# Kernel optimization log

Hardware: AMD Instinct MI355X
Metric: run time of the kernel (lower is better)

Reference implementation:

```python
import jax, jax.numpy as jnp
import numpy as np

EPS = 1e-5  # F.layer_norm default eps
H = 0.1     # step size h

def mm1(K, x):
    # 1x1 conv1d == channel matmul: K [O,I], x [B,I,M] -> [B,O,M]
    return jnp.einsum('oi,bim->bom', K, x)

def full_ln(x):
    # F.layer_norm(x, x.shape): normalize over ALL elements (incl. batch)
    m = jnp.mean(x)
    v = jnp.mean((x - m) ** 2)
    return (x - m) / jnp.sqrt(v + EPS)

def setup_inputs() -> dict:
    key = jax.random.key(0)
    ks = jax.random.split(key, 12)
    B, nNin, nEin = 1, 16, 16
    nNopen = nEopen = nEhid = nNclose = nEclose = 64
    nlayer, N, E = 4, 20000, 320000
    stdv, stdvp = 0.01, 0.001
    NEf = 2 * nNopen + nEopen   # 192
    Nnf = 2 * nEhid + nNopen    # 192
    return {
        'xn': jax.random.normal(ks[0], (B, nNin, N), jnp.float32),
        'xe': jax.random.normal(ks[1], (B, nEin, E), jnp.float32),
        'iInd': jax.random.randint(ks[2], (E,), 0, N, jnp.int32),
        'jInd': jax.random.randint(ks[3], (E,), 0, N, jnp.int32),
        'KNopen': jax.random.normal(ks[4], (nNopen, nNin), jnp.float32) * stdv,
        'KEopen': jax.random.normal(ks[5], (nEopen, nEin), jnp.float32) * stdv,
        'KNclose': jax.random.normal(ks[6], (nNclose, nNopen), jnp.float32) * stdv,
        'KEclose': jax.random.normal(ks[7], (nEclose, nEopen), jnp.float32) * stdv,
        'KE1': jax.random.uniform(ks[8], (nlayer, nEhid, NEf), jnp.float32) * stdvp,
        'KE2': jax.random.uniform(ks[9], (nlayer, nEhid, nEhid), jnp.float32) * stdvp,
        'KE3': jax.random.uniform(ks[10], (nlayer, nEopen, nEhid), jnp.float32) * stdvp,
        'KN': jax.random.uniform(ks[11], (nlayer, nNopen, Nnf), jnp.float32) * stdvp,
    }

def reference(xn, xe, iInd, jInd, KNopen, KEopen, KNclose, KEclose, KE1, KE2, KE3, KN):
    N = xn.shape[-1]
    xn = mm1(KNopen, xn)
    xe = mm1(KEopen, xe)
    nlayers = KE1.shape[0]
    for i in range(nlayers):
        xi = xn[:, :, iInd]
        xj = xn[:, :, jInd]
        gradX = xi - xj               # Graph.nodeGrad
        intX = 0.5 * (xi + xj)        # Graph.nodeAve
        xec = jnp.concatenate([intX, xe, gradX], axis=1)   # [B, 2*nNopen+nEopen, E]
        xec = jax.nn.relu(full_ln(mm1(KE1[i], xec)))
        xec = jax.nn.relu(full_ln(mm1(KE2[i], xec)))
        z = jnp.zeros(xec.shape[:2] + (N,), xec.dtype)
        divXe = z.at[:, :, iInd].add(xec).at[:, :, jInd].add(-xec)          # Graph.edgeDiv
        intXe = 0.5 * z.at[:, :, iInd].add(xec).at[:, :, jInd].add(xec)     # Graph.edgeAve
        xnc = jnp.concatenate([intXe, xn, divXe], axis=1)   # [B, 2*nEhid+nNopen, N]
        xe = xe + H * mm1(KE3[i], xec)
        xn = xn + H * mm1(KN[i], xnc)
    xn = mm1(KNclose, xn)
    xe = mm1(KEclose, xe)
    return (xn, xe)
```

## Files before the change

kernel.cpp:

```cpp
#include <hip/hip_runtime.h>
#include <math.h>

#define H_COEF 0.1f
#define LN_EPS 1e-5

__device__ __forceinline__ int lds_idx(int c, int el) {
  return (c << 8) + (el ^ c);
}

__device__ __forceinline__ void stat_reduce(float s, float ss, double* stat) {
#pragma unroll
  for (int off = 32; off > 0; off >>= 1) {
    s += __shfl_down(s, off);
    ss += __shfl_down(ss, off);
  }
  __shared__ float bs[8], bss[8];
  const int wid = threadIdx.x >> 6;
  const int lane = threadIdx.x & 63;
  if (lane == 0) { bs[wid] = s; bss[wid] = ss; }
  __syncthreads();
  if (threadIdx.x == 0) {
    float S = 0.f, SS = 0.f;
    const int nw = blockDim.x >> 6;
    for (int w = 0; w < nw; w++) { S += bs[w]; SS += bss[w]; }
    atomicAdd(stat, (double)S);
    atomicAdd(stat + 1, (double)SS);
  }
}

__global__ __launch_bounds__(256) void prep_weights_kernel(
    const float* __restrict__ KE1, const float* __restrict__ KN,
    const float* __restrict__ KNopen, const float* __restrict__ KNclose,
    float* __restrict__ WUT, float* __restrict__ WVT, float* __restrict__ WNaT,
    float* __restrict__ WNbT, float* __restrict__ WNcT,
    float* __restrict__ WNopT, float* __restrict__ WNclT, int nlayer) {
  const int idx = blockIdx.x * blockDim.x + threadIdx.x;
  const int total = nlayer * 4096;
  if (idx < total) {
    const int l = idx >> 12;
    const int r = idx & 4095;
    const int k = r >> 6;
    const int c = r & 63;
    const float a = KE1[(size_t)l * 12288 + c * 192 + k];
    const float g = KE1[(size_t)l * 12288 + c * 192 + 128 + k];
    WUT[idx] = 0.5f * a + g;
    WVT[idx] = 0.5f * a - g;
    WNaT[idx] = KN[(size_t)l * 12288 + c * 192 + k];
    WNbT[idx] = KN[(size_t)l * 12288 + c * 192 + 64 + k];
    WNcT[idx] = KN[(size_t)l * 12288 + c * 192 + 128 + k];
  }
  if (idx < 4096) {
    const int k = idx >> 6;
    const int c = idx & 63;
    WNclT[idx] = KNclose[c * 64 + k];
    if (k < 16) WNopT[k * 64 + c] = KNopen[c * 16 + k];
  }
}

__global__ __launch_bounds__(256) void hist_kernel(
    const int* __restrict__ iInd, const int* __restrict__ jInd,
    int* __restrict__ cnt_i, int* __restrict__ cnt_j, int E) {
  const int e = blockIdx.x * blockDim.x + threadIdx.x;
  if (e < E) {
    atomicAdd(&cnt_i[iInd[e]], 1);
    atomicAdd(&cnt_j[jInd[e]], 1);
  }
}

__global__ __launch_bounds__(1024) void scan_kernel(
    const int* __restrict__ cnt_i, const int* __restrict__ cnt_j,
    int* __restrict__ rowptr_i, int* __restrict__ cursor_i,
    int* __restrict__ rowptr_j, int* __restrict__ cursor_j, int N) {
  __shared__ int carry;
  __shared__ int tmp[1024];
  for (int pass = 0; pass < 2; ++pass) {
    const int* cnt = pass ? cnt_j : cnt_i;
    int* rp = pass ? rowptr_j : rowptr_i;
    int* cur = pass ? cursor_j : cursor_i;
    if (threadIdx.x == 0) carry = 0;
    __syncthreads();
    for (int base = 0; base < N; base += 1024) {
      const int idx = base + threadIdx.x;
      const int v = (idx < N) ? cnt[idx] : 0;
      tmp[threadIdx.x] = v;
      int acc = v;
      __syncthreads();
      for (int off = 1; off < 1024; off <<= 1) {
        const int add = (threadIdx.x >= off) ? tmp[threadIdx.x - off] : 0;
        __syncthreads();
        acc += add;
        tmp[threadIdx.x] = acc;
        __syncthreads();
      }
      const int excl = acc - v + carry;
      if (idx < N) { rp[idx] = excl; cur[idx] = excl; }
      __syncthreads();
      if (threadIdx.x == 1023) carry += tmp[1023];
      __syncthreads();
    }
    if (threadIdx.x == 0) rp[N] = carry;
    __syncthreads();
  }
}

__global__ __launch_bounds__(256) void fill_kernel(
    const int* __restrict__ iInd, const int* __restrict__ jInd,
    int* __restrict__ cursor_i, int* __restrict__ cursor_j,
    int* __restrict__ perm_i, int* __restrict__ perm_j, int E) {
  const int e = blockIdx.x * blockDim.x + threadIdx.x;
  if (e < E) {
    perm_i[atomicAdd(&cursor_i[iInd[e]], 1)] = e;
    perm_j[atomicAdd(&cursor_j[jInd[e]], 1)] = e;
  }
}

template <int KIN>
__global__ __launch_bounds__(256) void open_kernel(
    const float* __restrict__ W, const float* __restrict__ xin,
    float* __restrict__ out, int M) {
  const int e = blockIdx.x * blockDim.x + threadIdx.x;
  if (e >= M) return;
  float x[KIN];
#pragma unroll
  for (int k = 0; k < KIN; k++) x[k] = xin[(size_t)k * M + e];
#pragma unroll
  for (int c = 0; c < 64; c++) {
    float acc = 0.f;
#pragma unroll
    for (int k = 0; k < KIN; k++) acc += W[c * KIN + k] * x[k];
    out[(size_t)c * M + e] = acc;
  }
}

__global__ __launch_bounds__(256) void close_inplace_kernel(
    const float* __restrict__ W, float* x, int M) {
  const int e = blockIdx.x * blockDim.x + threadIdx.x;
  if (e >= M) return;
  float xv[64];
#pragma unroll
  for (int k = 0; k < 64; k++) xv[k] = x[(size_t)k * M + e];
#pragma unroll
  for (int c = 0; c < 64; c++) {
    float acc = 0.f;
#pragma unroll
    for (int k = 0; k < 64; k++) acc += W[c * 64 + k] * xv[k];
    x[(size_t)c * M + e] = acc;
  }
}

__global__ __launch_bounds__(256) void open_node_kernel(
    const float* __restrict__ WNopT, const float* __restrict__ xn_in,
    float* __restrict__ xn_node, int N) {
  const int n = blockIdx.x * 4 + (threadIdx.x >> 6);
  const int c = threadIdx.x & 63;
  if (n >= N) return;
  const float xv = (c < 16) ? xn_in[(size_t)c * N + n] : 0.f;
  float acc = 0.f;
#pragma unroll
  for (int k = 0; k < 16; k++) {
    const float xk = __shfl(xv, k);
    acc += WNopT[k * 64 + c] * xk;
  }
  xn_node[(size_t)n * 64 + c] = acc;
}

__global__ __launch_bounds__(256) void close_node_kernel(
    const float* __restrict__ WNclT, const float* __restrict__ xn_node,
    float* __restrict__ out, int N) {
  const int n = blockIdx.x * 4 + (threadIdx.x >> 6);
  const int c = threadIdx.x & 63;
  if (n >= N) return;
  const float xv = xn_node[(size_t)n * 64 + c];
  float acc = 0.f;
#pragma unroll
  for (int k = 0; k < 64; k++) {
    const float xk = __shfl(xv, k);
    acc += WNclT[k * 64 + c] * xk;
  }
  out[(size_t)c * N + n] = acc;
}

__global__ __launch_bounds__(256) void uv_kernel(
    const float* __restrict__ WUT, const float* __restrict__ WVT,
    const float* __restrict__ xn_node, float* __restrict__ U,
    float* __restrict__ V, int N) {
  const int n = blockIdx.x * 4 + (threadIdx.x >> 6);
  const int c = threadIdx.x & 63;
  if (n >= N) return;
  const float xv = xn_node[(size_t)n * 64 + c];
  float ua = 0.f, va = 0.f;
#pragma unroll
  for (int k = 0; k < 64; k++) {
    const float xk = __shfl(xv, k);
    ua += WUT[k * 64 + c] * xk;
    va += WVT[k * 64 + c] * xk;
  }
  U[(size_t)n * 64 + c] = ua;
  V[(size_t)n * 64 + c] = va;
}

__global__ __launch_bounds__(256) void edge1_kernel(
    const float* __restrict__ KE1_l, const float* __restrict__ xe,
    const float* __restrict__ U, const float* __restrict__ V,
    const int* __restrict__ iInd, const int* __restrict__ jInd,
    float* __restrict__ y, double* __restrict__ stat, int E) {
  __shared__ float sbuf[16384];
  const int t = threadIdx.x;
  const int base = blockIdx.x * 256;
  const int e = base + t;
  const bool full = (base + 256 <= E);
  float s = 0.f, ss = 0.f;
  if (e < E) {
    const int vi = iInd[e];
    const int vj = jInd[e];
    const float4* Up = (const float4*)(U + (size_t)vi * 64);
    const float4* Vp = (const float4*)(V + (size_t)vj * 64);
    float x[64];
#pragma unroll
    for (int k = 0; k < 64; k++) x[k] = xe[(size_t)k * E + e];
#pragma unroll
    for (int q = 0; q < 16; q++) {
      float4 uq = Up[q];
      float4 vq = Vp[q];
      const float* up = (const float*)&uq;
      const float* vp = (const float*)&vq;
#pragma unroll
      for (int u = 0; u < 4; u++) {
        const int c = q * 4 + u;
        const float* row = KE1_l + c * 192 + 64;
        float acc = up[u] + vp[u];
#pragma unroll
        for (int k = 0; k < 64; k++) acc += row[k] * x[k];
        s += acc;
        ss += acc * acc;
        if (full) sbuf[lds_idx(c, t)] = acc;
        else y[(size_t)e * 64 + c] = acc;
      }
    }
  }
  if (full) {
    __syncthreads();
    float4* dst = (float4*)(y + (size_t)base * 64);
#pragma unroll
    for (int it = 0; it < 16; it++) {
      const int f4 = t + it * 256;
      const int el = f4 >> 4;
      const int cb = (f4 & 15) << 2;
      float4 r;
      r.x = sbuf[lds_idx(cb + 0, el)];
      r.y = sbuf[lds_idx(cb + 1, el)];
      r.z = sbuf[lds_idx(cb + 2, el)];
      r.w = sbuf[lds_idx(cb + 3, el)];
      dst[f4] = r;
    }
  }
  stat_reduce(s, ss, stat);
}

__global__ __launch_bounds__(256) void edge2_kernel(
    const float* __restrict__ W, float* y, const double* __restrict__ statIn,
    double* __restrict__ statOut, double inv_n, int E) {
  __shared__ float sbuf[16384];
  const int t = threadIdx.x;
  const int base = blockIdx.x * 256;
  const int e = base + t;
  const bool full = (base + 256 <= E);
  float s = 0.f, ss = 0.f;
  if (full) {
    const float4* src = (const float4*)(y + (size_t)base * 64);
#pragma unroll
    for (int it = 0; it < 16; it++) {
      const int f4 = t + it * 256;
      const int el = f4 >> 4;
      const int cb = (f4 & 15) << 2;
      float4 r = src[f4];
      sbuf[lds_idx(cb + 0, el)] = r.x;
      sbuf[lds_idx(cb + 1, el)] = r.y;
      sbuf[lds_idx(cb + 2, el)] = r.z;
      sbuf[lds_idx(cb + 3, el)] = r.w;
    }
    __syncthreads();
  }
  if (e < E) {
    const double m = statIn[0] * inv_n;
    const double v = statIn[1] * inv_n - m * m;
    const float fm = (float)m;
    const float finv = (float)(1.0 / sqrt(v + LN_EPS));
    float tv[64];
    if (full) {
#pragma unroll
      for (int c = 0; c < 64; c++) {
        const float val = (sbuf[lds_idx(c, t)] - fm) * finv;
        tv[c] = val > 0.f ? val : 0.f;
      }
    } else {
#pragma unroll
      for (int c = 0; c < 64; c++) {
        const float val = (y[(size_t)e * 64 + c] - fm) * finv;
        tv[c] = val > 0.f ? val : 0.f;
      }
    }
#pragma unroll
    for (int c = 0; c < 64; c++) {
      float acc = 0.f;
#pragma unroll
      for (int k = 0; k < 64; k++) acc += W[c * 64 + k] * tv[k];
      s += acc;
      ss += acc * acc;
      if (full) sbuf[lds_idx(c, t)] = acc;
      else y[(size_t)e * 64 + c] = acc;
    }
  }
  if (full) {
    __syncthreads();
    float4* dst = (float4*)(y + (size_t)base * 64);
#pragma unroll
    for (int it = 0; it < 16; it++) {
      const int f4 = t + it * 256;
      const int el = f4 >> 4;
      const int cb = (f4 & 15) << 2;
      float4 r;
      r.x = sbuf[lds_idx(cb + 0, el)];
      r.y = sbuf[lds_idx(cb + 1, el)];
      r.z = sbuf[lds_idx(cb + 2, el)];
      r.w = sbuf[lds_idx(cb + 3, el)];
      dst[f4] = r;
    }
  }
  stat_reduce(s, ss, statOut);
}

__global__ __launch_bounds__(256) void edge3_kernel(
    const float* __restrict__ W, const float* __restrict__ y, float* xe,
    const double* __restrict__ statIn, double inv_n, int E) {
  const int e = blockIdx.x * blockDim.x + threadIdx.x;
  if (e >= E) return;
  const double m = statIn[0] * inv_n;
  const double v = statIn[1] * inv_n - m * m;
  const float fm = (float)m;
  const float finv = (float)(1.0 / sqrt(v + LN_EPS));
  float tv[64];
  const float4* yrow = (const float4*)(y + (size_t)e * 64);
#pragma unroll
  for (int q = 0; q < 16; q++) {
    float4 r = yrow[q];
    const float* rp = (const float*)&r;
#pragma unroll
    for (int u = 0; u < 4; u++) {
      const float val = (rp[u] - fm) * finv;
      tv[q * 4 + u] = val > 0.f ? val : 0.f;
    }
  }
#pragma unroll
  for (int c = 0; c < 64; c++) {
    float acc = 0.f;
#pragma unroll
    for (int k = 0; k < 64; k++) acc += W[c * 64 + k] * tv[k];
    xe[(size_t)c * E + e] += H_COEF * acc;
  }
}

__global__ __launch_bounds__(256) void fused_node_kernel(
    const float* __restrict__ y, const int* __restrict__ rowptr_i,
    const int* __restrict__ perm_i, const int* __restrict__ rowptr_j,
    const int* __restrict__ perm_j, const float* __restrict__ WNaT,
    const float* __restrict__ WNbT, const float* __restrict__ WNcT,
    float* __restrict__ xn_node, const double* __restrict__ statIn,
    double inv_n, int N) {
  const int n = blockIdx.x * 4 + (threadIdx.x >> 6);
  const int c = threadIdx.x & 63;
  if (n >= N) return;
  const double m = statIn[0] * inv_n;
  const double v = statIn[1] * inv_n - m * m;
  const float fm = (float)m;
  const float finv = (float)(1.0 / sqrt(v + LN_EPS));

  float si = 0.f;
  const int ib = rowptr_i[n], ie = rowptr_i[n + 1];
  for (int p = ib; p < ie; ++p) {
    const float val = (y[(size_t)perm_i[p] * 64 + c] - fm) * finv;
    si += val > 0.f ? val : 0.f;
  }
  float sj = 0.f;
  const int jb = rowptr_j[n], je = rowptr_j[n + 1];
  for (int p = jb; p < je; ++p) {
    const float val = (y[(size_t)perm_j[p] * 64 + c] - fm) * finv;
    sj += val > 0.f ? val : 0.f;
  }

  const float xv = xn_node[(size_t)n * 64 + c];
  const float a = 0.5f * (si + sj);
  const float d = si - sj;
  float acc = 0.f;
#pragma unroll
  for (int k = 0; k < 64; k++) {
    const float ak = __shfl(a, k);
    const float xk = __shfl(xv, k);
    const float dk = __shfl(d, k);
    acc += WNaT[k * 64 + c] * ak;
    acc += WNbT[k * 64 + c] * xk;
    acc += WNcT[k * 64 + c] * dk;
  }
  xn_node[(size_t)n * 64 + c] = xv + H_COEF * acc;
}

extern "C" void kernel_launch(void* const* d_in, const int* in_sizes, int n_in,
                              void* d_out, int out_size, void* d_ws,
                              size_t ws_size, hipStream_t stream) {
  const float* xn_in = (const float*)d_in[0];
  const float* xe_in = (const float*)d_in[1];
  const int* iInd = (const int*)d_in[2];
  const int* jInd = (const int*)d_in[3];
  const float* KNopen = (const float*)d_in[4];
  const float* KEopen = (const float*)d_in[5];
  const float* KNclose = (const float*)d_in[6];
  const float* KEclose = (const float*)d_in[7];
  const float* KE1 = (const float*)d_in[8];
  const float* KE2 = (const float*)d_in[9];
  const float* KE3 = (const float*)d_in[10];
  const float* KN = (const float*)d_in[11];

  const int N = in_sizes[0] / 16;
  const int E = in_sizes[2];
  const int nlayer = in_sizes[8] / (64 * 192);

  float* out = (float*)d_out;
  float* xn_out = out;
  float* xe = out + (size_t)64 * N;

  float* ws = (float*)d_ws;
  float* y = ws;
  float* U = y + (size_t)64 * E;
  float* V = U + (size_t)64 * N;
  float* xn_node = V + (size_t)64 * N;
  float* WUT = xn_node + (size_t)64 * N;
  float* WVT = WUT + (size_t)4096 * nlayer;
  float* WNaT = WVT + (size_t)4096 * nlayer;
  float* WNbT = WNaT + (size_t)4096 * nlayer;
  float* WNcT = WNbT + (size_t)4096 * nlayer;
  float* WNopT = WNcT + (size_t)4096 * nlayer;
  float* WNclT = WNopT + 1024;
  double* stat = (double*)(WNclT + 4096);
  int* cnt_i = (int*)(stat + 4 * nlayer);
  int* cnt_j = cnt_i + N;
  int* rowptr_i = cnt_j + N;
  int* cursor_i = rowptr_i + (N + 1);
  int* rowptr_j = cursor_i + N;
  int* cursor_j = rowptr_j + (N + 1);
  int* perm_i = cursor_j + N;
  int* perm_j = perm_i + E;

  const int be = (E + 255) / 256;
  const int bw = (N + 3) / 4;
  const double inv_n = 1.0 / (64.0 * (double)E);

  hipMemsetAsync(stat, 0, (size_t)nlayer * 4 * sizeof(double), stream);
  hipMemsetAsync(cnt_i, 0, (size_t)2 * N * sizeof(int), stream);

  prep_weights_kernel<<<(nlayer * 4096 + 255) / 256, 256, 0, stream>>>(
      KE1, KN, KNopen, KNclose, WUT, WVT, WNaT, WNbT, WNcT, WNopT, WNclT,
      nlayer);

  hist_kernel<<<be, 256, 0, stream>>>(iInd, jInd, cnt_i, cnt_j, E);
  scan_kernel<<<1, 1024, 0, stream>>>(cnt_i, cnt_j, rowptr_i, cursor_i,
                                      rowptr_j, cursor_j, N);
  fill_kernel<<<be, 256, 0, stream>>>(iInd, jInd, cursor_i, cursor_j, perm_i,
                                      perm_j, E);

  open_node_kernel<<<bw, 256, 0, stream>>>(WNopT, xn_in, xn_node, N);
  open_kernel<16><<<be, 256, 0, stream>>>(KEopen, xe_in, xe, E);

  for (int l = 0; l < nlayer; l++) {
    const float* KE1_l = KE1 + (size_t)l * 64 * 192;
    const float* KE2_l = KE2 + (size_t)l * 64 * 64;
    const float* KE3_l = KE3 + (size_t)l * 64 * 64;
    double* st1 = stat + (size_t)l * 4;
    double* st2 = st1 + 2;

    uv_kernel<<<bw, 256, 0, stream>>>(WUT + (size_t)l * 4096,
                                      WVT + (size_t)l * 4096, xn_node, U, V, N);
    edge1_kernel<<<be, 256, 0, stream>>>(KE1_l, xe, U, V, iInd, jInd, y, st1,
                                         E);
    edge2_kernel<<<be, 256, 0, stream>>>(KE2_l, y, st1, st2, inv_n, E);
    edge3_kernel<<<be, 256, 0, stream>>>(KE3_l, y, xe, st2, inv_n, E);
    fused_node_kernel<<<bw, 256, 0, stream>>>(
        y, rowptr_i, perm_i, rowptr_j, perm_j, WNaT + (size_t)l * 4096,
        WNbT + (size_t)l * 4096, WNcT + (size_t)l * 4096, xn_node, st2, inv_n,
        N);
  }

  close_node_kernel<<<bw, 256, 0, stream>>>(WNclT, xn_node, xn_out, N);
  close_inplace_kernel<<<be, 256, 0, stream>>>(KEclose, xe, E);
}
```

Measured before the change: 2.164 ms.

## Fuse open/uv/close stages into neighbors and chunk edge matmuls by 16 channels

Folds the edge open projection into the first edge1 pass, merges node open with the first U/V projection, and moves the per-layer U/V projection and the final node close into the fused node kernel, which removes several launches and a round of node and edge traffic. Edge kernels now compute outputs in 16-channel chunks with a smaller 4096-float LDS staging buffer, so register and LDS pressure drop and occupancy can rise, at the cost of extra barriers. edge2 now reads rows directly instead of staging the whole tile through LDS. The two prefix scans are merged into one 64-bit packed scan.

```diff
diff --git a/kernel.cpp b/kernel.cpp
--- a/kernel.cpp
+++ b/kernel.cpp
@@ -4,8 +4,8 @@
 #define H_COEF 0.1f
 #define LN_EPS 1e-5
 
-__device__ __forceinline__ int lds_idx(int c, int el) {
-  return (c << 8) + (el ^ c);
+__device__ __forceinline__ int lds_idx16(int c, int el) {
+  return (c << 8) + (el ^ ((c >> 2) << 3));
 }
 
 __device__ __forceinline__ void stat_reduce(float s, float ss, double* stat) {
@@ -71,35 +71,43 @@
     const int* __restrict__ cnt_i, const int* __restrict__ cnt_j,
     int* __restrict__ rowptr_i, int* __restrict__ cursor_i,
     int* __restrict__ rowptr_j, int* __restrict__ cursor_j, int N) {
-  __shared__ int carry;
-  __shared__ int tmp[1024];
-  for (int pass = 0; pass < 2; ++pass) {
-    const int* cnt = pass ? cnt_j : cnt_i;
-    int* rp = pass ? rowptr_j : rowptr_i;
-    int* cur = pass ? cursor_j : cursor_i;
-    if (threadIdx.x == 0) carry = 0;
+  __shared__ unsigned long long carry;
+  __shared__ unsigned long long tmp[1024];
+  if (threadIdx.x == 0) carry = 0ull;
+  __syncthreads();
+  for (int base = 0; base < N; base += 1024) {
+    const int idx = base + threadIdx.x;
+    unsigned long long v = 0ull;
+    if (idx < N)
+      v = (unsigned long long)(unsigned)cnt_i[idx] |
+          ((unsigned long long)(unsigned)cnt_j[idx] << 32);
+    tmp[threadIdx.x] = v;
+    unsigned long long acc = v;
     __syncthreads();
-    for (int base = 0; base < N; base += 1024) {
-      const int idx = base + threadIdx.x;
-      const int v = (idx < N) ? cnt[idx] : 0;
-      tmp[threadIdx.x] = v;
-      int acc = v;
+    for (int off = 1; off < 1024; off <<= 1) {
+      const unsigned long long add =
+          (threadIdx.x >= (unsigned)off) ? tmp[threadIdx.x - off] : 0ull;
       __syncthreads();
-      for (int off = 1; off < 1024; off <<= 1) {
-        const int add = (threadIdx.x >= off) ? tmp[threadIdx.x - off] : 0;
-        __syncthreads();
-        acc += add;
-        tmp[threadIdx.x] = acc;
-        __syncthreads();
-      }
-      const int excl = acc - v + carry;
-      if (idx < N) { rp[idx] = excl; cur[idx] = excl; }
+      acc += add;
+      tmp[threadIdx.x] = acc;
       __syncthreads();
-      if (threadIdx.x == 1023) carry += tmp[1023];
-      __syncthreads();
-    }
-    if (threadIdx.x == 0) rp[N] = carry;
+    }
+    const unsigned long long excl = acc - v + carry;
+    if (idx < N) {
+      const int lo = (int)(excl & 0xffffffffull);
+      const int hi = (int)(excl >> 32);
+      rowptr_i[idx] = lo;
+      cursor_i[idx] = lo;
+      rowptr_j[idx] = hi;
+      cursor_j[idx] = hi;
+    }
     __syncthreads();
+    if (threadIdx.x == 1023) carry += tmp[1023];
+    __syncthreads();
+  }
+  if (threadIdx.x == 0) {
+    rowptr_i[N] = (int)(carry & 0xffffffffull);
+    rowptr_j[N] = (int)(carry >> 32);
   }
 }
 
@@ -114,225 +122,190 @@
   }
 }
 
-template <int KIN>
-__global__ __launch_bounds__(256) void open_kernel(
-    const float* __restrict__ W, const float* __restrict__ xin,
-    float* __restrict__ out, int M) {
-  const int e = blockIdx.x * blockDim.x + threadIdx.x;
-  if (e >= M) return;
-  float x[KIN];
-#pragma unroll
-  for (int k = 0; k < KIN; k++) x[k] = xin[(size_t)k * M + e];
-#pragma unroll
-  for (int c = 0; c < 64; c++) {
-    float acc = 0.f;
-#pragma unroll
-    for (int k = 0; k < KIN; k++) acc += W[c * KIN + k] * x[k];
-    out[(size_t)c * M + e] = acc;
-  }
-}
-
-__global__ __launch_bounds__(256) void close_inplace_kernel(
-    const float* __restrict__ W, float* x, int M) {
-  const int e = blockIdx.x * blockDim.x + threadIdx.x;
-  if (e >= M) return;
-  float xv[64];
-#pragma unroll
-  for (int k = 0; k < 64; k++) xv[k] = x[(size_t)k * M + e];
-#pragma unroll
-  for (int c = 0; c < 64; c++) {
-    float acc = 0.f;
-#pragma unroll
-    for (int k = 0; k < 64; k++) acc += W[c * 64 + k] * xv[k];
-    x[(size_t)c * M + e] = acc;
-  }
-}
-
-__global__ __launch_bounds__(256) void open_node_kernel(
+__global__ __launch_bounds__(256) void open_node_uv_kernel(
     const float* __restrict__ WNopT, const float* __restrict__ xn_in,
-    float* __restrict__ xn_node, int N) {
+    const float* __restrict__ WUT0, const float* __restrict__ WVT0,
+    float* __restrict__ xn_node, float* __restrict__ U, float* __restrict__ V,
+    int N) {
   const int n = blockIdx.x * 4 + (threadIdx.x >> 6);
   const int c = threadIdx.x & 63;
   if (n >= N) return;
   const float xv = (c < 16) ? xn_in[(size_t)c * N + n] : 0.f;
   float acc = 0.f;
 #pragma unroll
-  for (int k = 0; k < 16; k++) {
-    const float xk = __shfl(xv, k);
-    acc += WNopT[k * 64 + c] * xk;
-  }
+  for (int k = 0; k < 16; k++) acc += WNopT[k * 64 + c] * __shfl(xv, k);
   xn_node[(size_t)n * 64 + c] = acc;
-}
-
-__global__ __launch_bounds__(256) void close_node_kernel(
-    const float* __restrict__ WNclT, const float* __restrict__ xn_node,
-    float* __restrict__ out, int N) {
-  const int n = blockIdx.x * 4 + (threadIdx.x >> 6);
-  const int c = threadIdx.x & 63;
-  if (n >= N) return;
-  const float xv = xn_node[(size_t)n * 64 + c];
-  float acc = 0.f;
+  float ua = 0.f, va = 0.f;
 #pragma unroll
   for (int k = 0; k < 64; k++) {
-    const float xk = __shfl(xv, k);
-    acc += WNclT[k * 64 + c] * xk;
-  }
-  out[(size_t)c * N + n] = acc;
-}
-
-__global__ __launch_bounds__(256) void uv_kernel(
-    const float* __restrict__ WUT, const float* __restrict__ WVT,
-    const float* __restrict__ xn_node, float* __restrict__ U,
-    float* __restrict__ V, int N) {
-  const int n = blockIdx.x * 4 + (threadIdx.x >> 6);
-  const int c = threadIdx.x & 63;
-  if (n >= N) return;
-  const float xv = xn_node[(size_t)n * 64 + c];
-  float ua = 0.f, va = 0.f;
-#pragma unroll
-  for (int k = 0; k < 64; k++) {
-    const float xk = __shfl(xv, k);
-    ua += WUT[k * 64 + c] * xk;
-    va += WVT[k * 64 + c] * xk;
+    const float xk = __shfl(acc, k);
+    ua += WUT0[k * 64 + c] * xk;
+    va += WVT0[k * 64 + c] * xk;
   }
   U[(size_t)n * 64 + c] = ua;
   V[(size_t)n * 64 + c] = va;
 }
 
+template <bool FIRST>
 __global__ __launch_bounds__(256) void edge1_kernel(
-    const float* __restrict__ KE1_l, const float* __restrict__ xe,
+    const float* __restrict__ KE1_l, const float* __restrict__ KEopen,
+    const float* __restrict__ xe_in, float* __restrict__ xe,
     const float* __restrict__ U, const float* __restrict__ V,
     const int* __restrict__ iInd, const int* __restrict__ jInd,
     float* __restrict__ y, double* __restrict__ stat, int E) {
-  __shared__ float sbuf[16384];
+  __shared__ float sbuf[4096];
   const int t = threadIdx.x;
   const int base = blockIdx.x * 256;
   const int e = base + t;
   const bool full = (base + 256 <= E);
   float s = 0.f, ss = 0.f;
+  float xcol[64];
+  int vi = 0, vj = 0;
   if (e < E) {
-    const int vi = iInd[e];
-    const int vj = jInd[e];
-    const float4* Up = (const float4*)(U + (size_t)vi * 64);
-    const float4* Vp = (const float4*)(V + (size_t)vj * 64);
-    float x[64];
-#pragma unroll
-    for (int k = 0; k < 64; k++) x[k] = xe[(size_t)k * E + e];
-#pragma unroll
-    for (int q = 0; q < 16; q++) {
-      float4 uq = Up[q];
-      float4 vq = Vp[q];
-      const float* up = (const float*)&uq;
-      const float* vp = (const float*)&vq;
-#pragma unroll
-      for (int u = 0; u < 4; u++) {
-        const int c = q * 4 + u;
-        const float* row = KE1_l + c * 192 + 64;
-        float acc = up[u] + vp[u];
-#pragma unroll
-        for (int k = 0; k < 64; k++) acc += row[k] * x[k];
-        s += acc;
-        ss += acc * acc;
-        if (full) sbuf[lds_idx(c, t)] = acc;
-        else y[(size_t)e * 64 + c] = acc;
-      }
-    }
-  }
-  if (full) {
-    __syncthreads();
-    float4* dst = (float4*)(y + (size_t)base * 64);
-#pragma unroll
-    for (int it = 0; it < 16; it++) {
-      const int f4 = t + it * 256;
-      const int el = f4 >> 4;
-      const int cb = (f4 & 15) << 2;
-      float4 r;
-      r.x = sbuf[lds_idx(cb + 0, el)];
-      r.y = sbuf[lds_idx(cb + 1, el)];
-      r.z = sbuf[lds_idx(cb + 2, el)];
-      r.w = sbuf[lds_idx(cb + 3, el)];
-      dst[f4] = r;
+    vi = iInd[e];
+    vj = jInd[e];
+    if (FIRST) {
+      float xin[16];
+#pragma unroll
+      for (int k = 0; k < 16; k++) xin[k] = xe_in[(size_t)k * E + e];
+#pragma unroll
+      for (int cc = 0; cc < 64; cc++) {
+        float a = 0.f;
+#pragma unroll
+        for (int k = 0; k < 16; k++) a += KEopen[cc * 16 + k] * xin[k];
+        xcol[cc] = a;
+        xe[(size_t)cc * E + e] = a;
+      }
+    } else {
+#pragma unroll
+      for (int k = 0; k < 64; k++) xcol[k] = xe[(size_t)k * E + e];
+    }
+  }
+  const float4* Up = (const float4*)(U + (size_t)vi * 64);
+  const float4* Vp = (const float4*)(V + (size_t)vj * 64);
+  for (int cb = 0; cb < 4; cb++) {
+    float acc[16];
+    if (e < E) {
+#pragma unroll
+      for (int q = 0; q < 4; q++) {
+        const float4 uq = Up[cb * 4 + q];
+        const float4 vq = Vp[cb * 4 + q];
+        acc[q * 4 + 0] = uq.x + vq.x;
+        acc[q * 4 + 1] = uq.y + vq.y;
+        acc[q * 4 + 2] = uq.z + vq.z;
+        acc[q * 4 + 3] = uq.w + vq.w;
+      }
+#pragma unroll
+      for (int cc = 0; cc < 16; cc++) {
+        const float* row = KE1_l + (cb * 16 + cc) * 192 + 64;
+        float a = acc[cc];
+#pragma unroll
+        for (int k = 0; k < 64; k++) a += row[k] * xcol[k];
+        acc[cc] = a;
+        s += a;
+        ss += a * a;
+      }
+    }
+    if (full) {
+#pragma unroll
+      for (int cc = 0; cc < 16; cc++) sbuf[lds_idx16(cc, t)] = acc[cc];
+      __syncthreads();
+      float4* dst = (float4*)(y + (size_t)base * 64);
+#pragma unroll
+      for (int it = 0; it < 4; it++) {
+        const int f4 = t + it * 256;
+        const int el = f4 >> 2;
+        const int qq = f4 & 3;
+        float4 r;
+        r.x = sbuf[lds_idx16(qq * 4 + 0, el)];
+        r.y = sbuf[lds_idx16(qq * 4 + 1, el)];
+        r.z = sbuf[lds_idx16(qq * 4 + 2, el)];
+        r.w = sbuf[lds_idx16(qq * 4 + 3, el)];
+        dst[(size_t)el * 16 + cb * 4 + qq] = r;
+      }
+      __syncthreads();
+    } else if (e < E) {
+#pragma unroll
+      for (int cc = 0; cc < 16; cc++)
+        y[(size_t)e * 64 + cb * 16 + cc] = acc[cc];
     }
   }
   stat_reduce(s, ss, stat);
 }
 
 __global__ __launch_bounds__(256) void edge2_kernel(
-    const float* __restrict__ W, float* y, const double* __restrict__ statIn,
-    double* __restrict__ statOut, double inv_n, int E) {
-  __shared__ float sbuf[16384];
+    const float* __restrict__ W, float* __restrict__ y,
+    const double* __restrict__ statIn, double* __restrict__ statOut,
+    double inv_n, int E) {
+  __shared__ float sbuf[4096];
   const int t = threadIdx.x;
   const int base = blockIdx.x * 256;
   const int e = base + t;
   const bool full = (base + 256 <= E);
   float s = 0.f, ss = 0.f;
-  if (full) {
-    const float4* src = (const float4*)(y + (size_t)base * 64);
-#pragma unroll
-    for (int it = 0; it < 16; it++) {
-      const int f4 = t + it * 256;
-      const int el = f4 >> 4;
-      const int cb = (f4 & 15) << 2;
-      float4 r = src[f4];
-      sbuf[lds_idx(cb + 0, el)] = r.x;
-      sbuf[lds_idx(cb + 1, el)] = r.y;
-      sbuf[lds_idx(cb + 2, el)] = r.z;
-      sbuf[lds_idx(cb + 3, el)] = r.w;
-    }
-    __syncthreads();
-  }
+  float tv[64];
   if (e < E) {
     const double m = statIn[0] * inv_n;
     const double v = statIn[1] * inv_n - m * m;
     const float fm = (float)m;
     const float finv = (float)(1.0 / sqrt(v + LN_EPS));
-    float tv[64];
+    const float4* yrow = (const float4*)(y + (size_t)e * 64);
+#pragma unroll
+    for (int q = 0; q < 16; q++) {
+      const float4 r = yrow[q];
+      const float* rp = (const float*)&r;
+#pragma unroll
+      for (int u = 0; u < 4; u++) {
+        const float val = (rp[u] - fm) * finv;
+        tv[q * 4 + u] = val > 0.f ? val : 0.f;
+      }
+    }
+  }
+  for (int cb = 0; cb < 4; cb++) {
+    float acc[16];
+    if (e < E) {
+#pragma unroll
+      for (int cc = 0; cc < 16; cc++) {
+        const float* row = W + (cb * 16 + cc) * 64;
+        float a = 0.f;
+#pragma unroll
+        for (int k = 0; k < 64; k++) a += row[k] * tv[k];
+        acc[cc] = a;
+        s += a;
+        ss += a * a;
+      }
+    }
     if (full) {
 #pragma unroll
-      for (int c = 0; c < 64; c++) {
-        const float val = (sbuf[lds_idx(c, t)] - fm) * finv;
-        tv[c] = val > 0.f ? val : 0.f;
-      }
-    } else {
-#pragma unroll
-      for (int c = 0; c < 64; c++) {
-        const float val = (y[(size_t)e * 64 + c] - fm) * finv;
-        tv[c] = val > 0.f ? val : 0.f;
-      }
-    }
-#pragma unroll
-    for (int c = 0; c < 64; c++) {
-      float acc = 0.f;
-#pragma unroll
-      for (int k = 0; k < 64; k++) acc += W[c * 64 + k] * tv[k];
-      s += acc;
-      ss += acc * acc;
-      if (full) sbuf[lds_idx(c, t)] = acc;
-      else y[(size_t)e * 64 + c] = acc;
-    }
-  }
-  if (full) {
-    __syncthreads();
-    float4* dst = (float4*)(y + (size_t)base * 64);
-#pragma unroll
-    for (int it = 0; it < 16; it++) {
-      const int f4 = t + it * 256;
-      const int el = f4 >> 4;
-      const int cb = (f4 & 15) << 2;
-      float4 r;
-      r.x = sbuf[lds_idx(cb + 0, el)];
-      r.y = sbuf[lds_idx(cb + 1, el)];
-      r.z = sbuf[lds_idx(cb + 2, el)];
-      r.w = sbuf[lds_idx(cb + 3, el)];
-      dst[f4] = r;
+      for (int cc = 0; cc < 16; cc++) sbuf[lds_idx16(cc, t)] = acc[cc];
+      __syncthreads();
+      float4* dst = (float4*)(y + (size_t)base * 64);
+#pragma unroll
+      for (int it = 0; it < 4; it++) {
+        const int f4 = t + it * 256;
+        const int el = f4 >> 2;
+        const int qq = f4 & 3;
+        float4 r;
+        r.x = sbuf[lds_idx16(qq * 4 + 0, el)];
+        r.y = sbuf[lds_idx16(qq * 4 + 1, el)];
+        r.z = sbuf[lds_idx16(qq * 4 + 2, el)];
+        r.w = sbuf[lds_idx16(qq * 4 + 3, el)];
+        dst[(size_t)el * 16 + cb * 4 + qq] = r;
+      }
+      __syncthreads();
+    } else if (e < E) {
+#pragma unroll
+      for (int cc = 0; cc < 16; cc++)
+        y[(size_t)e * 64 + cb * 16 + cc] = acc[cc];
     }
   }
   stat_reduce(s, ss, statOut);
 }
 
 __global__ __launch_bounds__(256) void edge3_kernel(
-    const float* __restrict__ W, const float* __restrict__ y, float* xe,
-    const double* __restrict__ statIn, double inv_n, int E) {
+    const float* __restrict__ W, const float* __restrict__ y,
+    float* __restrict__ xe, const double* __restrict__ statIn, double inv_n,
+    int E) {
   const int e = blockIdx.x * blockDim.x + threadIdx.x;
   if (e >= E) return;
   const double m = statIn[0] * inv_n;
@@ -343,7 +316,7 @@
   const float4* yrow = (const float4*)(y + (size_t)e * 64);
 #pragma unroll
   for (int q = 0; q < 16; q++) {
-    float4 r = yrow[q];
+    const float4 r = yrow[q];
     const float* rp = (const float*)&r;
 #pragma unroll
     for (int u = 0; u < 4; u++) {
@@ -351,22 +324,57 @@
       tv[q * 4 + u] = val > 0.f ? val : 0.f;
     }
   }
-#pragma unroll
-  for (int c = 0; c < 64; c++) {
-    float acc = 0.f;
-#pragma unroll
-    for (int k = 0; k < 64; k++) acc += W[c * 64 + k] * tv[k];
-    xe[(size_t)c * E + e] += H_COEF * acc;
-  }
-}
-
+  for (int cb = 0; cb < 4; cb++) {
+    float acc[16];
+#pragma unroll
+    for (int cc = 0; cc < 16; cc++) {
+      const float* row = W + (cb * 16 + cc) * 64;
+      float a = 0.f;
+#pragma unroll
+      for (int k = 0; k < 64; k++) a += row[k] * tv[k];
+      acc[cc] = a;
+    }
+#pragma unroll
+    for (int cc = 0; cc < 16; cc++) {
+      const size_t off = (size_t)(cb * 16 + cc) * E + e;
+      xe[off] += H_COEF * acc[cc];
+    }
+  }
+}
+
+__global__ __launch_bounds__(256) void close_edge_kernel(
+    const float* __restrict__ W, float* __restrict__ x, int M) {
+  const int e = blockIdx.x * blockDim.x + threadIdx.x;
+  if (e >= M) return;
+  float xv[64];
+#pragma unroll
+  for (int k = 0; k < 64; k++) xv[k] = x[(size_t)k * M + e];
+  for (int cb = 0; cb < 4; cb++) {
+    float acc[16];
+#pragma unroll
+    for (int cc = 0; cc < 16; cc++) {
+      const float* row = W + (cb * 16 + cc) * 64;
+      float a = 0.f;
+#pragma unroll
+      for (int k = 0; k < 64; k++) a += row[k] * xv[k];
+      acc[cc] = a;
+    }
+#pragma unroll
+    for (int cc = 0; cc < 16; cc++)
+      x[(size_t)(cb * 16 + cc) * M + e] = acc[cc];
+  }
+}
+
+template <bool FINAL>
 __global__ __launch_bounds__(256) void fused_node_kernel(
     const float* __restrict__ y, const int* __restrict__ rowptr_i,
     const int* __restrict__ perm_i, const int* __restrict__ rowptr_j,
     const int* __restrict__ perm_j, const float* __restrict__ WNaT,
     const float* __restrict__ WNbT, const float* __restrict__ WNcT,
-    float* __restrict__ xn_node, const double* __restrict__ statIn,
-    double inv_n, int N) {
+    const float* __restrict__ WUTn, const float* __restrict__ WVTn,
+    const float* __restrict__ WNclT, float* __restrict__ xn_node,
+    float* __restrict__ U, float* __restrict__ V, float* __restrict__ xn_out,
+    const double* __restrict__ statIn, double inv_n, int N) {
   const int n = blockIdx.x * 4 + (threadIdx.x >> 6);
   const int c = threadIdx.x & 63;
   if (n >= N) return;
@@ -401,7 +409,24 @@
     acc += WNbT[k * 64 + c] * xk;
     acc += WNcT[k * 64 + c] * dk;
   }
-  xn_node[(size_t)n * 64 + c] = xv + H_COEF * acc;
+  const float xn_new = xv + H_COEF * acc;
+  if (FINAL) {
+    float o = 0.f;
+#pragma unroll
+    for (int k = 0; k < 64; k++) o += WNclT[k * 64 + c] * __shfl(xn_new, k);
+    xn_out[(size_t)c * N + n] = o;
+  } else {
+    xn_node[(size_t)n * 64 + c] = xn_new;
+    float ua = 0.f, va = 0.f;
+#pragma unroll
+    for (int k = 0; k < 64; k++) {
+      const float xk = __shfl(xn_new, k);
+      ua += WUTn[k * 64 + c] * xk;
+      va += WVTn[k * 64 + c] * xk;
+    }
+    U[(size_t)n * 64 + c] = ua;
+    V[(size_t)n * 64 + c] = va;
+  }
 }
 
 extern "C" void kernel_launch(void* const* d_in, const int* in_sizes, int n_in,
@@ -467,8 +492,8 @@
   fill_kernel<<<be, 256, 0, stream>>>(iInd, jInd, cursor_i, cursor_j, perm_i,
                                       perm_j, E);
 
-  open_node_kernel<<<bw, 256, 0, stream>>>(WNopT, xn_in, xn_node, N);
-  open_kernel<16><<<be, 256, 0, stream>>>(KEopen, xe_in, xe, E);
+  open_node_uv_kernel<<<bw, 256, 0, stream>>>(WNopT, xn_in, WUT, WVT, xn_node,
+                                              U, V, N);
 
   for (int l = 0; l < nlayer; l++) {
     const float* KE1_l = KE1 + (size_t)l * 64 * 192;
@@ -476,19 +501,30 @@
     const float* KE3_l = KE3 + (size_t)l * 64 * 64;
     double* st1 = stat + (size_t)l * 4;
     double* st2 = st1 + 2;
-
-    uv_kernel<<<bw, 256, 0, stream>>>(WUT + (size_t)l * 4096,
-                                      WVT + (size_t)l * 4096, xn_node, U, V, N);
-    edge1_kernel<<<be, 256, 0, stream>>>(KE1_l, xe, U, V, iInd, jInd, y, st1,
-                                         E);
+    const bool last = (l == nlayer - 1);
+
+    if (l == 0) {
+      edge1_kernel<true><<<be, 256, 0, stream>>>(KE1_l, KEopen, xe_in, xe, U,
+                                                 V, iInd, jInd, y, st1, E);
+    } else {
+      edge1_kernel<false><<<be, 256, 0, stream>>>(KE1_l, KEopen, xe_in, xe, U,
+                                                  V, iInd, jInd, y, st1, E);
+    }
     edge2_kernel<<<be, 256, 0, stream>>>(KE2_l, y, st1, st2, inv_n, E);
     edge3_kernel<<<be, 256, 0, stream>>>(KE3_l, y, xe, st2, inv_n, E);
-    fused_node_kernel<<<bw, 256, 0, stream>>>(
-        y, rowptr_i, perm_i, rowptr_j, perm_j, WNaT + (size_t)l * 4096,
-        WNbT + (size_t)l * 4096, WNcT + (size_t)l * 4096, xn_node, st2, inv_n,
-        N);
-  }
-
-  close_node_kernel<<<bw, 256, 0, stream>>>(WNclT, xn_node, xn_out, N);
-  close_inplace_kernel<<<be, 256, 0, stream>>>(KEclose, xe, E);
-}
+    if (last) {
+      fused_node_kernel<true><<<bw, 256, 0, stream>>>(
+          y, rowptr_i, perm_i, rowptr_j, perm_j, WNaT + (size_t)l * 4096,
+          WNbT + (size_t)l * 4096, WNcT + (size_t)l * 4096, WUT, WVT, WNclT,
+          xn_node, U, V, xn_out, st2, inv_n, N);
+    } else {
+      fused_node_kernel<false><<<bw, 256, 0, stream>>>(
+          y, rowptr_i, perm_i, rowptr_j, perm_j, WNaT + (size_t)l * 4096,
+          WNbT + (size_t)l * 4096, WNcT + (size_t)l * 4096,
+          WUT + (size_t)(l + 1) * 4096, WVT + (size_t)(l + 1) * 4096, WNclT,
+          xn_node, U, V, xn_out, st2, inv_n, N);
+    }
+  }
+
+  close_edge_kernel<<<be, 256, 0, stream>>>(KEclose, xe, E);
+}
```

Measured after the change: 2.779 ms. 1.28x slower.
